# Performance work log

Hardware: AMD Instinct MI355X
Metric: run time of the kernel (lower is better)

The kernel has to match this reference:

```python
import jax, jax.numpy as jnp
import numpy as np

B = 256          # batch
T = 256          # block_size (tril mask requires seq_len == 256)
E = 384          # n_embed
H = 6            # n_head
HS = E // H      # head_size = 64
EPS = 1e-5       # torch LayerNorm default


def layernorm(x, g, b):
    m = x.mean(-1, keepdims=True)
    v = x.var(-1, keepdims=True)  # population variance, matches torch LN
    return (x - m) * jax.lax.rsqrt(v + EPS) * g + b


def setup_inputs() -> dict:
    key = jax.random.key(0)
    ks = jax.random.split(key, 8)
    s = lambda i, shape: jax.random.normal(ks[i], shape, jnp.float32) * 0.02
    return {
        "x": jax.random.normal(ks[0], (B, T, E), jnp.float32),
        # per-head Q/K/V linears (bias=False) packed along output dim: [E, H*HS]
        "Wq": s(1, (E, E)), "Wk": s(2, (E, E)), "Wv": s(3, (E, E)),
        "Wo": s(4, (E, E)), "bo": jnp.zeros((E,), jnp.float32),
        "W1": s(5, (E, 4 * E)), "b1": jnp.zeros((4 * E,), jnp.float32),
        "W2": s(6, (4 * E, E)), "b2": jnp.zeros((E,), jnp.float32),
        "g1": jnp.ones((E,), jnp.float32), "be1": jnp.zeros((E,), jnp.float32),
        "g2": jnp.ones((E,), jnp.float32), "be2": jnp.zeros((E,), jnp.float32),
    }


def reference(x, Wq, Wk, Wv, Wo, bo, W1, b1, W2, b2, g1, be1, g2, be2):
    # Block.forward: ffwd(ln2(sa(ln1(x)) + x)) + x   (dropout = identity at eval)
    h = layernorm(x, g1, be1)                                  # [B,T,E]
    q = (h @ Wq).reshape(B, T, H, HS)
    k = (h @ Wk).reshape(B, T, H, HS)
    v = (h @ Wv).reshape(B, T, H, HS)
    wei = jnp.einsum('bqhd,bkhd->bhqk', q, k) * (HS ** -0.5)   # [B,H,T,T]
    mask = jnp.tril(jnp.ones((T, T), dtype=bool))
    wei = jnp.where(mask, wei, -jnp.inf)
    wei = jax.nn.softmax(wei, axis=-1)
    attn = jnp.einsum('bhqk,bkhd->bqhd', wei, v).reshape(B, T, E)
    sa = attn @ Wo + bo                                        # output projection
    y = sa + x                                                 # residual 1
    h2 = layernorm(y, g2, be2)
    ff = jax.nn.relu(h2 @ W1 + b1) @ W2 + b2                   # FFN
    return ff + x                                              # residual 2 (to x!)
```

## Files before the change

### kernel.cpp

```cpp
#include <hip/hip_runtime.h>
#include <hip/hip_bf16.h>

typedef unsigned short bfu;
typedef __attribute__((ext_vector_type(8))) short short8;
typedef __attribute__((ext_vector_type(4))) float f32x4;

__device__ __forceinline__ bfu f2bf(float f) {
  return __builtin_bit_cast(bfu, __float2bfloat16(f));
}

__device__ __forceinline__ void gld16(const void* g, void* l) {
  __builtin_amdgcn_global_load_lds(
      (const __attribute__((address_space(1))) void*)g,
      (__attribute__((address_space(3))) void*)l, 16, 0, 0);
}

__device__ __forceinline__ int swz8(int row, int sl) {
  return (row << 7) + (((sl ^ (row & 7)) & 7) << 4);
}

__device__ __forceinline__ int swz(int row, int slot) {
  const int unit = row >> 1;
  const int s8 = ((row & 1) << 2) | slot;
  return (unit << 7) + (((s8 ^ unit) & 7) << 4) + ((s8 >> 3) << 7);
}
__device__ __forceinline__ void unswz(int p, int& row, int& colel) {
  const int unit = p >> 7;
  const int s8 = ((p >> 4) & 7) ^ (unit & 7);
  row = (unit << 1) | (s8 >> 2);
  colel = (s8 & 3) << 3;
}

__global__ void transpose_all(const float* __restrict__ Wq, const float* __restrict__ Wk,
                              const float* __restrict__ Wv, const float* __restrict__ Wo,
                              const float* __restrict__ W1, const float* __restrict__ W2,
                              bfu* __restrict__ wqkvT, bfu* __restrict__ woT,
                              bfu* __restrict__ w1T, bfu* __restrict__ w2T) {
  int idx = blockIdx.x * 256 + threadIdx.x;
  if (idx < 4 * 147456) {
    int r = idx / 147456, i = idx - r * 147456;
    int k = i / 384, n = i - k * 384;
    const float* W = r == 0 ? Wq : r == 1 ? Wk : r == 2 ? Wv : Wo;
    bfu* dst = r < 3 ? wqkvT + r * 147456 : woT;
    dst[n * 384 + k] = f2bf(W[i]);
  } else if (idx < 4 * 147456 + 589824) {
    int i = idx - 4 * 147456;
    int k = i / 1536, n = i - k * 1536;
    w1T[n * 384 + k] = f2bf(W1[i]);
  } else if (idx < 4 * 147456 + 2 * 589824) {
    int i = idx - 4 * 147456 - 589824;
    int k = i / 384, n = i - k * 384;
    w2T[(size_t)n * 1536 + k] = f2bf(W2[i]);
  }
}

__launch_bounds__(256)
__global__ void ln_kernel(const float* __restrict__ in, const float* __restrict__ g,
                          const float* __restrict__ be, bfu* __restrict__ out) {
  const int wv = threadIdx.x >> 6, ln = threadIdx.x & 63;
  const size_t row = (size_t)blockIdx.x * 4 + wv;
  const float* p = in + row * 384;
  float v[6], s = 0.f, ss = 0.f;
#pragma unroll
  for (int i = 0; i < 6; i++) { v[i] = p[i * 64 + ln]; s += v[i]; ss += v[i] * v[i]; }
#pragma unroll
  for (int m = 1; m < 64; m <<= 1) { s += __shfl_xor(s, m); ss += __shfl_xor(ss, m); }
  const float mean = s * (1.f / 384.f);
  const float rs = rsqrtf(ss * (1.f / 384.f) - mean * mean + 1e-5f);
  bfu* q = out + row * 384;
#pragma unroll
  for (int i = 0; i < 6; i++) {
    const int c = i * 64 + ln;
    q[c] = f2bf((v[i] - mean) * rs * g[c] + be[c]);
  }
}

template <int WM, int WN, int BIAS, int RELU, int RES, int OUTBF>
__launch_bounds__(512)
__global__ void gemm_ph(const bfu* __restrict__ A, const bfu* __restrict__ Bt,
                        const float* __restrict__ bias, const float* __restrict__ res,
                        void* __restrict__ Cout, int N, int K, int ntn) {
  constexpr int BM = WM * 32;
  constexpr int BN = WN * 64;
  constexpr int ACH = BM / 64;
  constexpr int BCH = BN / 64;
  __shared__ bfu sm[2][(BM + BN) * 64];
  const int tid = threadIdx.x;
  const int wv = tid >> 6, ln = tid & 63;
  const int cpx = gridDim.x >> 3;
  const int wg = (blockIdx.x & 7) * cpx + (blockIdx.x >> 3);
  const int bm = wg / ntn, bn = wg - bm * ntn;
  const int m0 = bm * BM, n0 = bn * BN;
  const int wr = wv >> 2, wc = wv & 3;
  const int fr = ln & 15, fslot = ln >> 4;
  const int lr = ln >> 3, lsl = (ln & 7) ^ lr;

  f32x4 acc[WM][WN];
#pragma unroll
  for (int i = 0; i < WM; i++)
#pragma unroll
    for (int j = 0; j < WN; j++) acc[i][j] = f32x4{0.f, 0.f, 0.f, 0.f};

  auto stageA = [&](int s, int kt) {
    char* smA = (char*)sm[s];
    const int col = (kt << 6) + (lsl << 3);
#pragma unroll
    for (int i = 0; i < ACH; ++i) {
      const int c = wv * ACH + i;
      gld16(A + (size_t)(m0 + (c << 3) + lr) * K + col, smA + (c << 10));
    }
  };
  auto stageB = [&](int s, int kt) {
    char* smB = (char*)sm[s] + BM * 128;
    const int col = (kt << 6) + (lsl << 3);
#pragma unroll
    for (int i = 0; i < BCH; ++i) {
      const int c = wv * BCH + i;
      gld16(Bt + (size_t)(n0 + (c << 3) + lr) * K + col, smB + (c << 10));
    }
  };

  const int nk = K >> 6;
  stageA(0, 0);
  stageB(0, 0);
  asm volatile("s_waitcnt vmcnt(0)" ::: "memory");
  __builtin_amdgcn_s_barrier();

  for (int kt = 0; kt < nk; ++kt) {
    const int cur = kt & 1;
    const char* smA = (const char*)sm[cur];
    const char* smB = smA + BM * 128;
    short8 bf[2][WN];
#pragma unroll
    for (int ph = 0; ph < 4; ++ph) {
      const int mh = ph >> 1, ks = ph & 1;
      short8 af[WM / 2];
#pragma unroll
      for (int i = 0; i < WM / 2; ++i)
        af[i] = *(const short8*)(smA +
            swz8(wr * (WM * 16) + (mh * (WM / 2) + i) * 16 + fr, ks * 4 + fslot));
      if (mh == 0) {
#pragma unroll
        for (int ni = 0; ni < WN; ++ni)
          bf[ks][ni] = *(const short8*)(smB +
              swz8(wc * (WN * 16) + ni * 16 + fr, ks * 4 + fslot));
      }
      if (kt + 1 < nk) {
        if (ph == 0) stageA(cur ^ 1, kt + 1);
        if (ph == 1) stageB(cur ^ 1, kt + 1);
      }
      __builtin_amdgcn_s_barrier();
      asm volatile("s_waitcnt lgkmcnt(0)" ::: "memory");
      __builtin_amdgcn_sched_barrier(0);
      __builtin_amdgcn_s_setprio(1);
#pragma unroll
      for (int i = 0; i < WM / 2; ++i)
#pragma unroll
        for (int ni = 0; ni < WN; ++ni)
          acc[mh * (WM / 2) + i][ni] = __builtin_amdgcn_mfma_f32_16x16x32_bf16(
              af[i], bf[ks][ni], acc[mh * (WM / 2) + i][ni], 0, 0, 0);
      __builtin_amdgcn_s_setprio(0);
      __builtin_amdgcn_s_barrier();
    }
    if (kt + 1 < nk) {
      asm volatile("s_waitcnt vmcnt(0)" ::: "memory");
      __builtin_amdgcn_s_barrier();
    }
  }

  const int rq = (ln >> 4) << 2;
#pragma unroll
  for (int mi = 0; mi < WM; mi++) {
#pragma unroll
    for (int ni = 0; ni < WN; ni++) {
      const int row = m0 + wr * (WM * 16) + mi * 16 + rq;
      const int col = n0 + wc * (WN * 16) + ni * 16 + fr;
      float bv = 0.f;
      if (BIAS) bv = bias[col];
#pragma unroll
      for (int r = 0; r < 4; r++) {
        float v = acc[mi][ni][r] + bv;
        if (RELU) v = fmaxf(v, 0.f);
        const size_t idx = (size_t)(row + r) * N + col;
        if (RES) v += res[idx];
        if (OUTBF) ((bfu*)Cout)[idx] = f2bf(v);
        else       ((float*)Cout)[idx] = v;
      }
    }
  }
}

__launch_bounds__(512)
__global__ void row_gemm(const bfu* __restrict__ A, const bfu* __restrict__ Bt,
                         const float* __restrict__ bias, const float* __restrict__ res,
                         const float* __restrict__ g, const float* __restrict__ be,
                         void* __restrict__ Cout, int K) {
  __shared__ bfu a_sm[4][128 * 32];
  __shared__ bfu b_sm[4][384 * 32];
  __shared__ float lnp[4][128][2];
  const int tid = threadIdx.x;
  const int wv = tid >> 6, ln = tid & 63;
  const int wr = wv >> 2, wc = wv & 3;
  const int fr = ln & 15, fslot = ln >> 4;
  const int m0 = blockIdx.x << 7;

  f32x4 acc[4][6];
#pragma unroll
  for (int i = 0; i < 4; i++)
#pragma unroll
    for (int j = 0; j < 6; j++) acc[i][j] = f32x4{0.f, 0.f, 0.f, 0.f};

  auto stage = [&](int buf, int kt) {
#pragma unroll
    for (int i = 0; i < 4; ++i) {
      const int c = wv * 4 + i;
      const int cc = (c < 8) ? c : (c - 8);
      const int p = cc * 1024 + (ln << 4);
      int r, colel;
      unswz(p, r, colel);
      const int col = kt * 32 + colel;
      if (c < 8)
        gld16(A + (size_t)(m0 + r) * K + col, (char*)a_sm[buf] + cc * 1024);
      else
        gld16(Bt + (size_t)r * K + col, (char*)b_sm[buf] + cc * 1024);
    }
  };

  const int nk = K >> 5;
#pragma unroll
  for (int i = 0; i < 3; ++i)
    if (i < nk) stage(i, i);

  for (int kt = 0; kt < nk; ++kt) {
    const int rem = nk - 1 - kt;
    if (rem >= 2)      asm volatile("s_waitcnt vmcnt(8)" ::: "memory");
    else if (rem == 1) asm volatile("s_waitcnt vmcnt(4)" ::: "memory");
    else               asm volatile("s_waitcnt vmcnt(0)" ::: "memory");
    __builtin_amdgcn_s_barrier();
    __builtin_amdgcn_sched_barrier(0);
    if (kt + 3 < nk) stage((kt + 3) & 3, kt + 3);
    const int cb = kt & 3;
    short8 af[4], bfr[6];
#pragma unroll
    for (int mi = 0; mi < 4; mi++)
      af[mi] = *(const short8*)((const char*)a_sm[cb] + swz(wr * 64 + mi * 16 + fr, fslot));
#pragma unroll
    for (int ni = 0; ni < 6; ni++)
      bfr[ni] = *(const short8*)((const char*)b_sm[cb] + swz(wc * 96 + ni * 16 + fr, fslot));
    __builtin_amdgcn_s_setprio(1);
#pragma unroll
    for (int mi = 0; mi < 4; mi++)
#pragma unroll
      for (int ni = 0; ni < 6; ni++)
        acc[mi][ni] = __builtin_amdgcn_mfma_f32_16x16x32_bf16(af[mi], bfr[ni], acc[mi][ni], 0, 0, 0);
    __builtin_amdgcn_s_setprio(0);
  }

  const int rq = (ln >> 4) << 2;
#pragma unroll
  for (int mi = 0; mi < 4; mi++) {
    const int row = wr * 64 + mi * 16 + rq;
#pragma unroll
    for (int ni = 0; ni < 6; ni++) {
      const int col = wc * 96 + ni * 16 + fr;
      const float bv = bias[col];
#pragma unroll
      for (int r = 0; r < 4; r++)
        acc[mi][ni][r] += bv + res[(size_t)(m0 + row + r) * 384 + col];
    }
  }

#pragma unroll
  for (int mi = 0; mi < 4; mi++) {
    float s[4] = {0.f, 0.f, 0.f, 0.f}, ss[4] = {0.f, 0.f, 0.f, 0.f};
#pragma unroll
    for (int ni = 0; ni < 6; ni++)
#pragma unroll
      for (int r = 0; r < 4; r++) {
        const float v = acc[mi][ni][r];
        s[r] += v; ss[r] += v * v;
      }
#pragma unroll
    for (int m = 1; m < 16; m <<= 1)
#pragma unroll
      for (int r = 0; r < 4; r++) {
        s[r] += __shfl_xor(s[r], m);
        ss[r] += __shfl_xor(ss[r], m);
      }
    if (fr == 0) {
#pragma unroll
      for (int r = 0; r < 4; r++) {
        lnp[wc][wr * 64 + mi * 16 + rq + r][0] = s[r];
        lnp[wc][wr * 64 + mi * 16 + rq + r][1] = ss[r];
      }
    }
  }
  __syncthreads();
#pragma unroll
  for (int mi = 0; mi < 4; mi++) {
#pragma unroll
    for (int r = 0; r < 4; r++) {
      const int row = wr * 64 + mi * 16 + rq + r;
      const float sm = lnp[0][row][0] + lnp[1][row][0] + lnp[2][row][0] + lnp[3][row][0];
      const float sq = lnp[0][row][1] + lnp[1][row][1] + lnp[2][row][1] + lnp[3][row][1];
      const float mean = sm * (1.f / 384.f);
      const float rs = rsqrtf(sq * (1.f / 384.f) - mean * mean + 1e-5f);
#pragma unroll
      for (int ni = 0; ni < 6; ni++) {
        const int col = wc * 96 + ni * 16 + fr;
        ((bfu*)Cout)[(size_t)(m0 + row) * 384 + col] =
            f2bf((acc[mi][ni][r] - mean) * rs * g[col] + be[col]);
      }
    }
  }
}

#define KPAD 72
#define VPAD 264
#define PPAD 264

__launch_bounds__(512)
__global__ void attn_kernel(const bfu* __restrict__ qkv, bfu* __restrict__ ob) {
  __shared__ bfu k_sm[256 * KPAD];
  __shared__ bfu vt_sm[64 * VPAD];
  __shared__ bfu p_sm[8 * 16 * PPAD];
  const int b = blockIdx.x / 6, h = blockIdx.x - b * 6;
  const int tid = threadIdx.x;
  const int wv = tid >> 6, ln = tid & 63;
  const int fr = ln & 15, fc = (ln >> 4) << 3;
  const size_t inbase = (size_t)b * 256 * 1152 + h * 64;
  const bfu* qb = qkv + inbase;
  const bfu* kb = qkv + inbase + 384;
  const bfu* vb = qkv + inbase + 768;
  const size_t obase = (size_t)b * 256 * 384 + h * 64;

  {
    const int row = tid >> 1;
    const int dh = (tid & 1) << 5;
    const bfu* kg = kb + (size_t)row * 1152 + dh;
    const bfu* vg = vb + (size_t)row * 1152 + dh;
#pragma unroll
    for (int i = 0; i < 4; i++) {
      short8 t8 = *(const short8*)(kg + i * 8);
      *(short8*)&k_sm[row * KPAD + dh + i * 8] = t8;
      short8 v8 = *(const short8*)(vg + i * 8);
#pragma unroll
      for (int j = 0; j < 8; j++)
        vt_sm[(dh + i * 8 + j) * VPAD + row] = (bfu)v8[j];
    }
  }
  __syncthreads();

  bfu* pw = &p_sm[wv * 16 * PPAD];
  const int rq = (ln >> 4) << 2;

#pragma unroll
  for (int si = 0; si < 2; ++si) {
    const int s = si ? (15 - wv) : wv;
    const int qr0 = s << 4;
    const int nf = s + 1;
    short8 aq[2];
#pragma unroll
    for (int dc = 0; dc < 2; dc++)
      aq[dc] = *(const short8*)(qb + (size_t)(qr0 + fr) * 1152 + dc * 32 + fc);

    f32x4 sacc[16];
#pragma unroll
    for (int f = 0; f < 16; f++) sacc[f] = f32x4{0.f, 0.f, 0.f, 0.f};
#pragma unroll
    for (int f = 0; f < 16; f++) if (f < nf) {
#pragma unroll
      for (int dc = 0; dc < 2; dc++) {
        short8 kf = *(const short8*)&k_sm[(f * 16 + fr) * KPAD + dc * 32 + fc];
        sacc[f] = __builtin_amdgcn_mfma_f32_16x16x32_bf16(aq[dc], kf, sacc[f], 0, 0, 0);
      }
    }
    float mr[4] = {-3e38f, -3e38f, -3e38f, -3e38f};
#pragma unroll
    for (int f = 0; f < 16; f++) if (f < nf) {
#pragma unroll
      for (int r = 0; r < 4; r++) {
        float sv = sacc[f][r] * 0.125f;
        if (f * 16 + fr > qr0 + rq + r) sv = -3e38f;
        sacc[f][r] = sv;
        mr[r] = fmaxf(mr[r], sv);
      }
    }
#pragma unroll
    for (int msk = 1; msk < 16; msk <<= 1) {
#pragma unroll
      for (int r = 0; r < 4; r++) mr[r] = fmaxf(mr[r], __shfl_xor(mr[r], msk));
    }
    float ls[4] = {0.f, 0.f, 0.f, 0.f};
#pragma unroll
    for (int f = 0; f < 16; f++) if (f < nf) {
#pragma unroll
      for (int r = 0; r < 4; r++) {
        float p = __expf(sacc[f][r] - mr[r]);
        sacc[f][r] = p;
        ls[r] += p;
      }
    }
#pragma unroll
    for (int msk = 1; msk < 16; msk <<= 1) {
#pragma unroll
      for (int r = 0; r < 4; r++) ls[r] += __shfl_xor(ls[r], msk);
    }
#pragma unroll
    for (int f = 0; f < 16; f++) if (f < nf) {
#pragma unroll
      for (int r = 0; r < 4; r++)
        pw[(rq + r) * PPAD + f * 16 + fr] = f2bf(sacc[f][r]);
    }
    if (nf & 1) {
#pragma unroll
      for (int r = 0; r < 4; r++) pw[(rq + r) * PPAD + nf * 16 + fr] = 0;
    }
    f32x4 oc[4];
#pragma unroll
    for (int n = 0; n < 4; n++) oc[n] = f32x4{0.f, 0.f, 0.f, 0.f};
    const int kcs = (nf + 1) >> 1;
#pragma unroll
    for (int kc = 0; kc < 8; ++kc) if (kc < kcs) {
      short8 pa = *(const short8*)&pw[fr * PPAD + kc * 32 + fc];
#pragma unroll
      for (int n = 0; n < 4; n++) {
        short8 vf = *(const short8*)&vt_sm[(n * 16 + fr) * VPAD + kc * 32 + fc];
        oc[n] = __builtin_amdgcn_mfma_f32_16x16x32_bf16(pa, vf, oc[n], 0, 0, 0);
      }
    }
    float inv[4];
#pragma unroll
    for (int r = 0; r < 4; r++) inv[r] = 1.f / ls[r];
#pragma unroll
    for (int n = 0; n < 4; n++) {
#pragma unroll
      for (int r = 0; r < 4; r++)
        ob[obase + (size_t)(qr0 + rq + r) * 384 + n * 16 + fr] = f2bf(oc[n][r] * inv[r]);
    }
  }
}

extern "C" void kernel_launch(void* const* d_in, const int* in_sizes, int n_in,
                              void* d_out, int out_size, void* d_ws, size_t ws_size,
                              hipStream_t stream) {
  const float* x   = (const float*)d_in[0];
  const float* Wq  = (const float*)d_in[1];
  const float* Wk  = (const float*)d_in[2];
  const float* Wv  = (const float*)d_in[3];
  const float* Wo  = (const float*)d_in[4];
  const float* bo  = (const float*)d_in[5];
  const float* W1  = (const float*)d_in[6];
  const float* b1  = (const float*)d_in[7];
  const float* W2  = (const float*)d_in[8];
  const float* b2  = (const float*)d_in[9];
  const float* g1  = (const float*)d_in[10];
  const float* be1 = (const float*)d_in[11];
  const float* g2  = (const float*)d_in[12];
  const float* be2 = (const float*)d_in[13];
  float* out = (float*)d_out;
  char* ws = (char*)d_ws;

  bfu* wqkvT = (bfu*)(ws + 0);
  bfu* woT   = (bfu*)(ws + 884736);
  bfu* w1T   = (bfu*)(ws + 1179648);
  bfu* w2T   = (bfu*)(ws + 2359296);
  char* H    = ws + 3538944;
  char* BIG  = H + 50331648;
  bfu* hb    = (bfu*)BIG;
  bfu* qkvb  = (bfu*)(BIG + 50331648);
  bfu* attnb = (bfu*)BIG;
  bfu* h2b   = (bfu*)H;
  bfu* ab    = (bfu*)BIG;

  transpose_all<<<6912, 256, 0, stream>>>(Wq, Wk, Wv, Wo, W1, W2, wqkvT, woT, w1T, w2T);

  ln_kernel<<<16384, 256, 0, stream>>>(x, g1, be1, hb);

  gemm_ph<8, 3, 0, 0, 0, 1><<<1536, 512, 0, stream>>>(hb, wqkvT, nullptr, nullptr, qkvb, 1152, 384, 6);

  attn_kernel<<<1536, 512, 0, stream>>>(qkvb, attnb);

  row_gemm<<<512, 512, 0, stream>>>(attnb, woT, bo, x, g2, be2, h2b, 384);

  gemm_ph<8, 4, 1, 1, 0, 1><<<1536, 512, 0, stream>>>(h2b, w1T, b1, nullptr, ab, 1536, 384, 6);

  gemm_ph<4, 6, 1, 0, 1, 0><<<512, 512, 0, stream>>>(ab, w2T, b2, x, out, 384, 1536, 1);
}
```

Baseline: 493.5 us.

## Fuse FFN up and down projections into one kernel keeping hidden tile in LDS

Replaces the two FFN GEMM launches with a single kernel that computes a 64-row tile of relu(h2@W1+b1) in 128-column chunks, stages each chunk in shared memory as bf16, and immediately multiplies it by the matching slice of W2, accumulating the output in registers. W1 and W2 are pre-laid out in MFMA-fragment order so each lane loads its B fragment directly from global memory. This avoids writing and re-reading the large 1536-wide intermediate activation through HBM. In exchange, weights are streamed straight from global or L2 with no LDS staging or double buffering, the tiles are smaller, and there are extra barriers per chunk. The gemm_ph template loses its bias, relu and residual options since only the QKV projection still uses it.

```diff
diff --git a/kernel.cpp b/kernel.cpp
--- a/kernel.cpp
+++ b/kernel.cpp
@@ -35,7 +35,7 @@
                               const float* __restrict__ Wv, const float* __restrict__ Wo,
                               const float* __restrict__ W1, const float* __restrict__ W2,
                               bfu* __restrict__ wqkvT, bfu* __restrict__ woT,
-                              bfu* __restrict__ w1T, bfu* __restrict__ w2T) {
+                              bfu* __restrict__ w1f, bfu* __restrict__ w2f) {
   int idx = blockIdx.x * 256 + threadIdx.x;
   if (idx < 4 * 147456) {
     int r = idx / 147456, i = idx - r * 147456;
@@ -46,11 +46,15 @@
   } else if (idx < 4 * 147456 + 589824) {
     int i = idx - 4 * 147456;
     int k = i / 1536, n = i - k * 1536;
-    w1T[n * 384 + k] = f2bf(W1[i]);
+    int di = (((n >> 4) * 12 + (k >> 5)) << 9) +
+             (((((k >> 3) & 3) << 4) | (n & 15)) << 3) + (k & 7);
+    w1f[di] = f2bf(W1[i]);
   } else if (idx < 4 * 147456 + 2 * 589824) {
     int i = idx - 4 * 147456 - 589824;
     int k = i / 384, n = i - k * 384;
-    w2T[(size_t)n * 1536 + k] = f2bf(W2[i]);
+    int di = (((n >> 4) * 48 + (k >> 5)) << 9) +
+             (((((k >> 3) & 3) << 4) | (n & 15)) << 3) + (k & 7);
+    w2f[di] = f2bf(W2[i]);
   }
 }
 
@@ -75,10 +79,112 @@
   }
 }
 
-template <int WM, int WN, int BIAS, int RELU, int RES, int OUTBF>
+__launch_bounds__(512)
+__global__ void ffn_fused(const bfu* __restrict__ h2, const bfu* __restrict__ w1f,
+                          const bfu* __restrict__ w2f, const float* __restrict__ b1,
+                          const float* __restrict__ b2, const float* __restrict__ x,
+                          float* __restrict__ out) {
+  __shared__ bfu h2s[64][392];
+  __shared__ bfu Ts[64][136];
+  const int tid = threadIdx.x, wv = tid >> 6, ln = tid & 63;
+  const int m0 = blockIdx.x << 6;
+  const int fr = ln & 15, fs = ln >> 4;
+  const int rq = fs << 2;
+  const int wr1 = wv >> 2, wc1 = wv & 3;
+  const int wr2 = wv >> 2, wc2 = wv & 3;
+
+  {
+    const int row = tid >> 3, seg = tid & 7;
+    const bfu* src = h2 + (size_t)(m0 + row) * 384 + seg * 48;
+    bfu* dst = &h2s[row][seg * 48];
+#pragma unroll
+    for (int i = 0; i < 6; i++)
+      *(short8*)(dst + i * 8) = *(const short8*)(src + i * 8);
+  }
+  __syncthreads();
+
+  f32x4 acc2[2][6];
+#pragma unroll
+  for (int i = 0; i < 2; i++)
+#pragma unroll
+    for (int j = 0; j < 6; j++) acc2[i][j] = f32x4{0.f, 0.f, 0.f, 0.f};
+
+  for (int c = 0; c < 12; ++c) {
+    f32x4 acc1[2][2];
+#pragma unroll
+    for (int i = 0; i < 2; i++)
+#pragma unroll
+      for (int j = 0; j < 2; j++) acc1[i][j] = f32x4{0.f, 0.f, 0.f, 0.f};
+#pragma unroll
+    for (int ks = 0; ks < 12; ++ks) {
+      short8 a1[2], bf1[2];
+#pragma unroll
+      for (int mi = 0; mi < 2; mi++)
+        a1[mi] = *(const short8*)&h2s[wr1 * 32 + mi * 16 + fr][ks * 32 + rq * 2];
+#pragma unroll
+      for (int ni = 0; ni < 2; ni++)
+        bf1[ni] = *(const short8*)(w1f +
+            ((size_t)((c * 8 + wc1 * 2 + ni) * 12 + ks) << 9) + (ln << 3));
+#pragma unroll
+      for (int mi = 0; mi < 2; mi++)
+#pragma unroll
+        for (int ni = 0; ni < 2; ni++)
+          acc1[mi][ni] = __builtin_amdgcn_mfma_f32_16x16x32_bf16(
+              a1[mi], bf1[ni], acc1[mi][ni], 0, 0, 0);
+    }
+    __syncthreads();
+#pragma unroll
+    for (int mi = 0; mi < 2; mi++) {
+#pragma unroll
+      for (int ni = 0; ni < 2; ni++) {
+        const int colc = wc1 * 32 + ni * 16 + fr;
+        const float bv = b1[c * 128 + colc];
+#pragma unroll
+        for (int r = 0; r < 4; r++) {
+          float v = fmaxf(acc1[mi][ni][r] + bv, 0.f);
+          Ts[wr1 * 32 + mi * 16 + rq + r][colc] = f2bf(v);
+        }
+      }
+    }
+    __syncthreads();
+#pragma unroll
+    for (int ks = 0; ks < 4; ++ks) {
+      short8 a2[2], bf2[6];
+#pragma unroll
+      for (int mi = 0; mi < 2; mi++)
+        a2[mi] = *(const short8*)&Ts[wr2 * 32 + mi * 16 + fr][ks * 32 + rq * 2];
+#pragma unroll
+      for (int ni = 0; ni < 6; ni++)
+        bf2[ni] = *(const short8*)(w2f +
+            ((size_t)((wc2 * 6 + ni) * 48 + c * 4 + ks) << 9) + (ln << 3));
+#pragma unroll
+      for (int mi = 0; mi < 2; mi++)
+#pragma unroll
+        for (int ni = 0; ni < 6; ni++)
+          acc2[mi][ni] = __builtin_amdgcn_mfma_f32_16x16x32_bf16(
+              a2[mi], bf2[ni], acc2[mi][ni], 0, 0, 0);
+    }
+  }
+
+#pragma unroll
+  for (int mi = 0; mi < 2; mi++) {
+#pragma unroll
+    for (int ni = 0; ni < 6; ni++) {
+      const int col = wc2 * 96 + ni * 16 + fr;
+      const float bv = b2[col];
+#pragma unroll
+      for (int r = 0; r < 4; r++) {
+        const int row = m0 + wr2 * 32 + mi * 16 + rq + r;
+        const size_t idx = (size_t)row * 384 + col;
+        out[idx] = acc2[mi][ni][r] + bv + x[idx];
+      }
+    }
+  }
+}
+
+template <int WM, int WN, int OUTBF>
 __launch_bounds__(512)
 __global__ void gemm_ph(const bfu* __restrict__ A, const bfu* __restrict__ Bt,
-                        const float* __restrict__ bias, const float* __restrict__ res,
                         void* __restrict__ Cout, int N, int K, int ntn) {
   constexpr int BM = WM * 32;
   constexpr int BN = WN * 64;
@@ -175,14 +281,10 @@
     for (int ni = 0; ni < WN; ni++) {
       const int row = m0 + wr * (WM * 16) + mi * 16 + rq;
       const int col = n0 + wc * (WN * 16) + ni * 16 + fr;
-      float bv = 0.f;
-      if (BIAS) bv = bias[col];
-#pragma unroll
-      for (int r = 0; r < 4; r++) {
-        float v = acc[mi][ni][r] + bv;
-        if (RELU) v = fmaxf(v, 0.f);
+#pragma unroll
+      for (int r = 0; r < 4; r++) {
+        float v = acc[mi][ni][r];
         const size_t idx = (size_t)(row + r) * N + col;
-        if (RES) v += res[idx];
         if (OUTBF) ((bfu*)Cout)[idx] = f2bf(v);
         else       ((float*)Cout)[idx] = v;
       }
@@ -463,27 +565,24 @@
 
   bfu* wqkvT = (bfu*)(ws + 0);
   bfu* woT   = (bfu*)(ws + 884736);
-  bfu* w1T   = (bfu*)(ws + 1179648);
-  bfu* w2T   = (bfu*)(ws + 2359296);
+  bfu* w1f   = (bfu*)(ws + 1179648);
+  bfu* w2f   = (bfu*)(ws + 2359296);
   char* H    = ws + 3538944;
   char* BIG  = H + 50331648;
   bfu* hb    = (bfu*)BIG;
   bfu* qkvb  = (bfu*)(BIG + 50331648);
   bfu* attnb = (bfu*)BIG;
   bfu* h2b   = (bfu*)H;
-  bfu* ab    = (bfu*)BIG;
-
-  transpose_all<<<6912, 256, 0, stream>>>(Wq, Wk, Wv, Wo, W1, W2, wqkvT, woT, w1T, w2T);
+
+  transpose_all<<<6912, 256, 0, stream>>>(Wq, Wk, Wv, Wo, W1, W2, wqkvT, woT, w1f, w2f);
 
   ln_kernel<<<16384, 256, 0, stream>>>(x, g1, be1, hb);
 
-  gemm_ph<8, 3, 0, 0, 0, 1><<<1536, 512, 0, stream>>>(hb, wqkvT, nullptr, nullptr, qkvb, 1152, 384, 6);
+  gemm_ph<8, 3, 1><<<1536, 512, 0, stream>>>(hb, wqkvT, qkvb, 1152, 384, 6);
 
   attn_kernel<<<1536, 512, 0, stream>>>(qkvb, attnb);
 
   row_gemm<<<512, 512, 0, stream>>>(attnb, woT, bo, x, g2, be2, h2b, 384);
 
-  gemm_ph<8, 4, 1, 1, 0, 1><<<1536, 512, 0, stream>>>(h2b, w1T, b1, nullptr, ab, 1536, 384, 6);
-
-  gemm_ph<4, 6, 1, 0, 1, 0><<<512, 512, 0, stream>>>(ab, w2T, b2, x, out, 384, 1536, 1);
-}
+  ffn_fused<<<1024, 512, 0, stream>>>(h2b, w1f, w2f, b1, b2, x, out);
+}
```

New measurement: 524.9 us. 6.4% more time.

## Replace double-buffered GEMM with triple-buffered 256x128 tile kernel

Applied to the files above, without the earlier changes.

Replaces the templated double-buffered GEMM with a fixed 256x128-tile kernel that uses a three-stage LDS ring, prefetching two K-steps ahead with partial vmcnt waits. Loads for the next-next stage are spread across four compute phases. Tile shapes change for all three GEMMs (smaller N tiles, more workgroups), aiming to hide global load latency better and improve occupancy on the W2 GEMM. Costs 144KB LDS per block, which limits residency to one block per CU, and lowers reuse of the A tile.

```diff
diff --git a/kernel.cpp b/kernel.cpp
--- a/kernel.cpp
+++ b/kernel.cpp
@@ -75,106 +75,105 @@
   }
 }
 
-template <int WM, int WN, int BIAS, int RELU, int RES, int OUTBF>
+template <int BIAS, int RELU, int RES, int OUTBF>
 __launch_bounds__(512)
-__global__ void gemm_ph(const bfu* __restrict__ A, const bfu* __restrict__ Bt,
-                        const float* __restrict__ bias, const float* __restrict__ res,
-                        void* __restrict__ Cout, int N, int K, int ntn) {
-  constexpr int BM = WM * 32;
-  constexpr int BN = WN * 64;
-  constexpr int ACH = BM / 64;
-  constexpr int BCH = BN / 64;
-  __shared__ bfu sm[2][(BM + BN) * 64];
+__global__ void gemm3b(const bfu* __restrict__ A, const bfu* __restrict__ Bt,
+                       const float* __restrict__ bias, const float* __restrict__ res,
+                       void* __restrict__ Cout, int N, int K, int ntn) {
+  __shared__ char sm[3 * 49152];
   const int tid = threadIdx.x;
   const int wv = tid >> 6, ln = tid & 63;
   const int cpx = gridDim.x >> 3;
   const int wg = (blockIdx.x & 7) * cpx + (blockIdx.x >> 3);
   const int bm = wg / ntn, bn = wg - bm * ntn;
-  const int m0 = bm * BM, n0 = bn * BN;
+  const int m0 = bm << 8, n0 = bn << 7;
   const int wr = wv >> 2, wc = wv & 3;
   const int fr = ln & 15, fslot = ln >> 4;
   const int lr = ln >> 3, lsl = (ln & 7) ^ lr;
 
-  f32x4 acc[WM][WN];
-#pragma unroll
-  for (int i = 0; i < WM; i++)
-#pragma unroll
-    for (int j = 0; j < WN; j++) acc[i][j] = f32x4{0.f, 0.f, 0.f, 0.f};
-
-  auto stageA = [&](int s, int kt) {
-    char* smA = (char*)sm[s];
+  f32x4 acc[8][2];
+#pragma unroll
+  for (int i = 0; i < 8; i++)
+#pragma unroll
+    for (int j = 0; j < 2; j++) acc[i][j] = f32x4{0.f, 0.f, 0.f, 0.f};
+
+  auto stageA = [&](int dbuf, int kt, int half) {
+    char* smA = sm + dbuf * 49152;
     const int col = (kt << 6) + (lsl << 3);
 #pragma unroll
-    for (int i = 0; i < ACH; ++i) {
-      const int c = wv * ACH + i;
+    for (int i = 0; i < 2; ++i) {
+      const int c = (wv << 2) + (half << 1) + i;
       gld16(A + (size_t)(m0 + (c << 3) + lr) * K + col, smA + (c << 10));
     }
   };
-  auto stageB = [&](int s, int kt) {
-    char* smB = (char*)sm[s] + BM * 128;
+  auto stageB = [&](int dbuf, int kt, int j) {
+    char* smB = sm + dbuf * 49152 + 32768;
     const int col = (kt << 6) + (lsl << 3);
-#pragma unroll
-    for (int i = 0; i < BCH; ++i) {
-      const int c = wv * BCH + i;
-      gld16(Bt + (size_t)(n0 + (c << 3) + lr) * K + col, smB + (c << 10));
-    }
+    const int c = (wv << 1) + j;
+    gld16(Bt + (size_t)(n0 + (c << 3) + lr) * K + col, smB + (c << 10));
   };
 
   const int nk = K >> 6;
-  stageA(0, 0);
-  stageB(0, 0);
-  asm volatile("s_waitcnt vmcnt(0)" ::: "memory");
+  stageA(0, 0, 0); stageA(0, 0, 1); stageB(0, 0, 0); stageB(0, 0, 1);
+  stageA(1, 1, 0); stageA(1, 1, 1); stageB(1, 1, 0); stageB(1, 1, 1);
+  asm volatile("s_waitcnt vmcnt(6)" ::: "memory");
   __builtin_amdgcn_s_barrier();
 
-  for (int kt = 0; kt < nk; ++kt) {
-    const int cur = kt & 1;
-    const char* smA = (const char*)sm[cur];
-    const char* smB = smA + BM * 128;
-    short8 bf[2][WN];
-#pragma unroll
-    for (int ph = 0; ph < 4; ++ph) {
-      const int mh = ph >> 1, ks = ph & 1;
-      short8 af[WM / 2];
-#pragma unroll
-      for (int i = 0; i < WM / 2; ++i)
-        af[i] = *(const short8*)(smA +
-            swz8(wr * (WM * 16) + (mh * (WM / 2) + i) * 16 + fr, ks * 4 + fslot));
-      if (mh == 0) {
-#pragma unroll
-        for (int ni = 0; ni < WN; ++ni)
-          bf[ks][ni] = *(const short8*)(smB +
-              swz8(wc * (WN * 16) + ni * 16 + fr, ks * 4 + fslot));
-      }
-      if (kt + 1 < nk) {
-        if (ph == 0) stageA(cur ^ 1, kt + 1);
-        if (ph == 1) stageB(cur ^ 1, kt + 1);
-      }
-      __builtin_amdgcn_s_barrier();
-      asm volatile("s_waitcnt lgkmcnt(0)" ::: "memory");
-      __builtin_amdgcn_sched_barrier(0);
-      __builtin_amdgcn_s_setprio(1);
-#pragma unroll
-      for (int i = 0; i < WM / 2; ++i)
-#pragma unroll
-        for (int ni = 0; ni < WN; ++ni)
-          acc[mh * (WM / 2) + i][ni] = __builtin_amdgcn_mfma_f32_16x16x32_bf16(
-              af[i], bf[ks][ni], acc[mh * (WM / 2) + i][ni], 0, 0, 0);
-      __builtin_amdgcn_s_setprio(0);
-      __builtin_amdgcn_s_barrier();
-    }
-    if (kt + 1 < nk) {
-      asm volatile("s_waitcnt vmcnt(0)" ::: "memory");
-      __builtin_amdgcn_s_barrier();
-    }
+  int cb = 0;
+  for (int k = 0; k < nk; ++k) {
+    const char* smA = sm + cb * 49152;
+    const char* smB = smA + 32768;
+    int sb = cb + 2; if (sb >= 3) sb -= 3;
+    const bool st = (k + 2) < nk;
+#pragma unroll
+    for (int mh = 0; mh < 2; ++mh) {
+      short8 af[4][2];
+#pragma unroll
+      for (int i = 0; i < 4; ++i)
+#pragma unroll
+        for (int ks = 0; ks < 2; ++ks)
+          af[i][ks] = *(const short8*)(smA +
+              swz8(wr * 128 + mh * 64 + i * 16 + fr, ks * 4 + fslot));
+#pragma unroll
+      for (int nh = 0; nh < 2; ++nh) {
+        short8 bf[2];
+#pragma unroll
+        for (int ks = 0; ks < 2; ++ks)
+          bf[ks] = *(const short8*)(smB + swz8(wc * 32 + nh * 16 + fr, ks * 4 + fslot));
+        if (st) {
+          if (mh == 0 && nh == 0) stageA(sb, k + 2, 0);
+          if (mh == 0 && nh == 1) stageA(sb, k + 2, 1);
+          if (mh == 1 && nh == 0) stageB(sb, k + 2, 0);
+          if (mh == 1 && nh == 1) stageB(sb, k + 2, 1);
+        }
+        __builtin_amdgcn_s_barrier();
+        asm volatile("s_waitcnt lgkmcnt(0)" ::: "memory");
+        __builtin_amdgcn_sched_barrier(0);
+        __builtin_amdgcn_s_setprio(1);
+#pragma unroll
+        for (int i = 0; i < 4; ++i)
+#pragma unroll
+          for (int ks = 0; ks < 2; ++ks)
+            acc[mh * 4 + i][nh] = __builtin_amdgcn_mfma_f32_16x16x32_bf16(
+                af[i][ks], bf[ks], acc[mh * 4 + i][nh], 0, 0, 0);
+        __builtin_amdgcn_s_setprio(0);
+        if (mh == 1 && nh == 1 && k + 1 < nk) {
+          if (st) asm volatile("s_waitcnt vmcnt(6)" ::: "memory");
+          else    asm volatile("s_waitcnt vmcnt(0)" ::: "memory");
+        }
+        __builtin_amdgcn_s_barrier();
+      }
+    }
+    cb = (cb + 1 == 3) ? 0 : cb + 1;
   }
 
   const int rq = (ln >> 4) << 2;
 #pragma unroll
-  for (int mi = 0; mi < WM; mi++) {
-#pragma unroll
-    for (int ni = 0; ni < WN; ni++) {
-      const int row = m0 + wr * (WM * 16) + mi * 16 + rq;
-      const int col = n0 + wc * (WN * 16) + ni * 16 + fr;
+  for (int mi = 0; mi < 8; mi++) {
+#pragma unroll
+    for (int ni = 0; ni < 2; ni++) {
+      const int row = m0 + wr * 128 + mi * 16 + rq;
+      const int col = n0 + wc * 32 + ni * 16 + fr;
       float bv = 0.f;
       if (BIAS) bv = bias[col];
 #pragma unroll
@@ -477,13 +476,13 @@
 
   ln_kernel<<<16384, 256, 0, stream>>>(x, g1, be1, hb);
 
-  gemm_ph<8, 3, 0, 0, 0, 1><<<1536, 512, 0, stream>>>(hb, wqkvT, nullptr, nullptr, qkvb, 1152, 384, 6);
+  gemm3b<0, 0, 0, 1><<<2304, 512, 0, stream>>>(hb, wqkvT, nullptr, nullptr, qkvb, 1152, 384, 9);
 
   attn_kernel<<<1536, 512, 0, stream>>>(qkvb, attnb);
 
   row_gemm<<<512, 512, 0, stream>>>(attnb, woT, bo, x, g2, be2, h2b, 384);
 
-  gemm_ph<8, 4, 1, 1, 0, 1><<<1536, 512, 0, stream>>>(h2b, w1T, b1, nullptr, ab, 1536, 384, 6);
-
-  gemm_ph<4, 6, 1, 0, 1, 0><<<512, 512, 0, stream>>>(ab, w2T, b2, x, out, 384, 1536, 1);
-}
+  gemm3b<1, 1, 0, 1><<<3072, 512, 0, stream>>>(h2b, w1T, b1, nullptr, ab, 1536, 384, 12);
+
+  gemm3b<1, 0, 1, 0><<<768, 512, 0, stream>>>(ab, w2T, b2, x, out, 384, 1536, 3);
+}
```

Measured after the change: 509.6 us. 1.03x slower.
